# Performance work log

Hardware: AMD Instinct MI355X
Metric: run time of the kernel (lower is better)

## Reference

```python
import jax, jax.numpy as jnp
import numpy as np


def _pointnet(x, w1, b1, w2, b2, w3, b3):
    # x: [B, P, 5] -> pointwise MLP then max-pool over points -> [B, 64]
    h = jax.nn.relu(x @ w1.T + b1)
    h = jax.nn.relu(h @ w2.T + b2)
    h = h @ w3.T + b3
    return h.max(axis=1)


def _lstm_layer(x, wih, whh, bih, bhh):
    # x: [B, T, D]; PyTorch gate order i, f, g, o
    B = x.shape[0]
    H = whh.shape[1]
    def step(carry, xt):
        h, c = carry
        g = xt @ wih.T + bih + h @ whh.T + bhh
        i, f, gg, o = jnp.split(g, 4, axis=-1)
        c = jax.nn.sigmoid(f) * c + jax.nn.sigmoid(i) * jnp.tanh(gg)
        h = jax.nn.sigmoid(o) * jnp.tanh(c)
        return (h, c), h
    init = (jnp.zeros((B, H), x.dtype), jnp.zeros((B, H), x.dtype))
    (h_last, _), hs = jax.lax.scan(step, init, jnp.swapaxes(x, 0, 1))
    return jnp.swapaxes(hs, 0, 1), h_last


def _edge_conv(h, mask, wt, bt, wp, bp):
    # DGL EdgeConv: h_i' = max_{j in N(i)} theta(h_j - h_i) + phi(h_i)
    # theta is linear -> max_j (Th_j) - Th_i + b_theta + phi(h_i)
    Th = h @ wt.T                       # [V,128]
    Ph = h @ wp.T + bp                  # [V,128]
    neigh_max = jnp.max(jnp.where(mask[:, :, None], Th[None, :, :], -jnp.inf), axis=1)
    return neigh_max - Th + bt + Ph


def _edge_regr(e, w1, b1, w2, b2):
    return jax.nn.sigmoid(jax.nn.relu(e @ w1.T + b1) @ w2.T + b2)


def _affinity(h, N, M, er_w1, er_b1, er_w2, er_b2):
    # faithful to source: edges[i*M+j] = h[j] - h[i]  (j indexes first M rows, as in the code)
    E = (h[None, :M, :] - h[:N, None, :]).reshape(N * M, -1)
    return _edge_regr(E, er_w1, er_b1, er_w2, er_b2).reshape(N, M)


def setup_inputs() -> dict:
    key = jax.random.key(0)
    ks = iter(jax.random.split(key, 40))
    N, M, P, T = 256, 256, 512, 10
    lin = lambda k, o, i: (jax.random.normal(k, (o, i), jnp.float32) / np.sqrt(i)).astype(jnp.float32)
    inp = {
        'det_pts': jax.random.normal(next(ks), (N, P, 5), jnp.float32),
        'det_boxes': jax.random.normal(next(ks), (N, 9), jnp.float32),
        'track_pts': jax.random.normal(next(ks), (M, P, 5), jnp.float32),
        'track_boxes': jax.random.normal(next(ks), (M, T, 9), jnp.float32),
        'adj': jax.random.randint(next(ks), (N + M, N + M), 0, 2, jnp.int32),
        'pn_w1': lin(next(ks), 64, 5), 'pn_b1': jnp.zeros((64,), jnp.float32),
        'pn_w2': lin(next(ks), 128, 64), 'pn_b2': jnp.zeros((128,), jnp.float32),
        'pn_w3': lin(next(ks), 64, 128), 'pn_b3': jnp.zeros((64,), jnp.float32),
        'dm_w1': lin(next(ks), 32, 9), 'dm_b1': jnp.zeros((32,), jnp.float32),
        'dm_w2': lin(next(ks), 64, 32), 'dm_b2': jnp.zeros((64,), jnp.float32),
        'l0_wih': lin(next(ks), 256, 9), 'l0_whh': lin(next(ks), 256, 64),
        'l0_bih': jnp.zeros((256,), jnp.float32), 'l0_bhh': jnp.zeros((256,), jnp.float32),
        'l1_wih': lin(next(ks), 256, 64), 'l1_whh': lin(next(ks), 256, 64),
        'l1_bih': jnp.zeros((256,), jnp.float32), 'l1_bhh': jnp.zeros((256,), jnp.float32),
        'gc_wt': jnp.stack([lin(next(ks), 128, 128) for _ in range(4)]),
        'gc_bt': jnp.zeros((4, 128), jnp.float32),
        'gc_wp': jnp.stack([lin(next(ks), 128, 128) for _ in range(4)]),
        'gc_bp': jnp.zeros((4, 128), jnp.float32),
        'er_w1': lin(next(ks), 64, 128), 'er_b1': jnp.zeros((64,), jnp.float32),
        'er_w2': lin(next(ks), 1, 64), 'er_b2': jnp.zeros((1,), jnp.float32),
    }
    return inp


def reference(det_pts, det_boxes, track_pts, track_boxes, adj,
              pn_w1, pn_b1, pn_w2, pn_b2, pn_w3, pn_b3,
              dm_w1, dm_b1, dm_w2, dm_b2,
              l0_wih, l0_whh, l0_bih, l0_bhh,
              l1_wih, l1_whh, l1_bih, l1_bhh,
              gc_wt, gc_bt, gc_wp, gc_bp,
              er_w1, er_b1, er_w2, er_b2):
    N, M = det_pts.shape[0], track_pts.shape[0]
    V = N + M
    # appearance features (shared PointNet)
    det_app = _pointnet(det_pts, pn_w1, pn_b1, pn_w2, pn_b2, pn_w3, pn_b3)    # [N,64]
    trk_app = _pointnet(track_pts, pn_w1, pn_b1, pn_w2, pn_b2, pn_w3, pn_b3)  # [M,64]
    # motion features
    det_mot = jax.nn.relu(det_boxes @ dm_w1.T + dm_b1) @ dm_w2.T + dm_b2      # [N,64]
    hs0, _ = _lstm_layer(track_boxes, l0_wih, l0_whh, l0_bih, l0_bhh)
    _, trk_mot = _lstm_layer(hs0, l1_wih, l1_whh, l1_bih, l1_bhh)             # [M,64]
    h = jnp.concatenate([
        jnp.concatenate([det_app, det_mot], axis=1),
        jnp.concatenate([trk_app, trk_mot], axis=1)], axis=0)                 # [V,128]
    # neighbor-source mask: edge i->j for adj[i,j]!=0, plus self-loops
    mask = (adj.T != 0) | jnp.eye(V, dtype=bool)                              # mask[i,j]: j is source neighbor of i
    aff1 = None
    for k in range(4):
        h = jax.nn.relu(_edge_conv(h, mask, gc_wt[k], gc_bt[k], gc_wp[k], gc_bp[k]))
        if k == 0:
            aff1 = _affinity(h, N, M, er_w1, er_b1, er_w2, er_b2)
    aff_final = _affinity(h, N, M, er_w1, er_b1, er_w2, er_b2)
    return jnp.stack([aff1, aff_final])  # [2, N, M]
```

## Files before the change

kernel.cpp:

```cpp
#include <hip/hip_runtime.h>
#include <math.h>

#define NDET 256
#define NTRK 256
#define NV   512
#define PPTS 512

typedef short bf16x8 __attribute__((ext_vector_type(8)));
typedef float f32x4  __attribute__((ext_vector_type(4)));

__device__ __forceinline__ float sigf(float x) { return 1.f / (1.f + expf(-x)); }

__device__ __forceinline__ short f2bf(float f) {
    unsigned u = __float_as_uint(f);
    u += 0x7fffu + ((u >> 16) & 1u);
    return (short)(u >> 16);
}
__device__ __forceinline__ unsigned pack2bf(float lo, float hi) {
    return (unsigned)(unsigned short)f2bf(lo) | ((unsigned)(unsigned short)f2bf(hi) << 16);
}

__global__ __launch_bounds__(256) void pointnet_kernel(
    const float* __restrict__ det_pts, const float* __restrict__ track_pts,
    const float* __restrict__ w1, const float* __restrict__ b1,
    const float* __restrict__ w2, const float* __restrict__ b2,
    const float* __restrict__ w3, const float* __restrict__ b3,
    const float* __restrict__ det_boxes,
    const float* __restrict__ dw1, const float* __restrict__ db1,
    const float* __restrict__ dw2, const float* __restrict__ db2,
    float* __restrict__ hout)
{
    __shared__ __align__(16) short sW2[128][72];
    __shared__ __align__(16) short sW3[64][136];
    __shared__ __align__(16) short sH1[64][72];
    __shared__ __align__(16) short sH2[64][136];
    __shared__ __align__(16) float sX[320];
    __shared__ float sW1f[64][6];
    __shared__ float sB1[64];
    __shared__ float sbox[9];
    __shared__ float sh32[32];

    const int t  = threadIdx.x;
    const int b  = blockIdx.x;
    const int w  = t >> 6;
    const int ln = t & 15;
    const int kq = (t >> 4) & 3;
    const float* x = (b < NDET) ? (det_pts + (size_t)b * PPTS * 5)
                                : (track_pts + (size_t)(b - NDET) * PPTS * 5);

    for (int i = t; i < 8192; i += 256) sW2[i >> 6][i & 63] = f2bf(w2[i]);
    for (int i = t; i < 8192; i += 256) sW3[i >> 7][i & 127] = f2bf(w3[i]);
    for (int i = t; i < 320; i += 256) sW1f[i / 5][i % 5] = w1[i];
    if (t < 64) sB1[t] = b1[t];
    __syncthreads();

    bf16x8 bf2[2][2];
#pragma unroll
    for (int nt = 0; nt < 2; ++nt)
#pragma unroll
        for (int Kt = 0; Kt < 2; ++Kt)
            bf2[nt][Kt] = *(const bf16x8*)&sW2[32 * w + 16 * nt + ln][kq * 8 + 32 * Kt];
    bf16x8 bf3[4];
#pragma unroll
    for (int Kt = 0; Kt < 4; ++Kt)
        bf3[Kt] = *(const bf16x8*)&sW3[16 * w + ln][kq * 8 + 32 * Kt];
    float bn[2];
#pragma unroll
    for (int nt = 0; nt < 2; ++nt) bn[nt] = b2[32 * w + 16 * nt + ln];

    float runmax[4] = {-1e30f, -1e30f, -1e30f, -1e30f};

    const int pt = t & 63;
    for (int c = 0; c < PPTS / 64; ++c) {
        for (int i = t; i < 320; i += 256) sX[i] = x[c * 320 + i];
        __syncthreads();

        {
            float xv[5];
#pragma unroll
            for (int k = 0; k < 5; ++k) xv[k] = sX[pt * 5 + k];
#pragma unroll
            for (int jj = 0; jj < 8; ++jj) {
                const int d0 = w * 16 + 2 * jj;
                float a0 = sB1[d0], a1 = sB1[d0 + 1];
#pragma unroll
                for (int k = 0; k < 5; ++k) {
                    a0 = fmaf(xv[k], sW1f[d0][k], a0);
                    a1 = fmaf(xv[k], sW1f[d0 + 1][k], a1);
                }
                *(unsigned*)&sH1[pt][d0] = pack2bf(fmaxf(a0, 0.f), fmaxf(a1, 0.f));
            }
        }
        __syncthreads();

        {
            bf16x8 af[4][2];
#pragma unroll
            for (int Mt = 0; Mt < 4; ++Mt)
#pragma unroll
                for (int Kt = 0; Kt < 2; ++Kt)
                    af[Mt][Kt] = *(const bf16x8*)&sH1[16 * Mt + ln][kq * 8 + 32 * Kt];
#pragma unroll
            for (int Mt = 0; Mt < 4; ++Mt) {
#pragma unroll
                for (int nt = 0; nt < 2; ++nt) {
                    f32x4 cacc = {0.f, 0.f, 0.f, 0.f};
                    cacc = __builtin_amdgcn_mfma_f32_16x16x32_bf16(af[Mt][0], bf2[nt][0], cacc, 0, 0, 0);
                    cacc = __builtin_amdgcn_mfma_f32_16x16x32_bf16(af[Mt][1], bf2[nt][1], cacc, 0, 0, 0);
                    const int col = 32 * w + 16 * nt + ln;
#pragma unroll
                    for (int r = 0; r < 4; ++r)
                        sH2[16 * Mt + kq * 4 + r][col] = f2bf(fmaxf(cacc[r] + bn[nt], 0.f));
                }
            }
        }
        __syncthreads();

        {
#pragma unroll
            for (int Mt = 0; Mt < 4; ++Mt) {
                f32x4 cacc = {0.f, 0.f, 0.f, 0.f};
#pragma unroll
                for (int Kt = 0; Kt < 4; ++Kt) {
                    const bf16x8 a = *(const bf16x8*)&sH2[16 * Mt + ln][kq * 8 + 32 * Kt];
                    cacc = __builtin_amdgcn_mfma_f32_16x16x32_bf16(a, bf3[Kt], cacc, 0, 0, 0);
                }
#pragma unroll
                for (int r = 0; r < 4; ++r) runmax[r] = fmaxf(runmax[r], cacc[r]);
            }
        }
        __syncthreads();
    }

    float rm = fmaxf(fmaxf(runmax[0], runmax[1]), fmaxf(runmax[2], runmax[3]));
    rm = fmaxf(rm, __shfl_xor(rm, 16));
    rm = fmaxf(rm, __shfl_xor(rm, 32));
    if ((t & 63) < 16) {
        const int n = 16 * w + ln;
        hout[b * 128 + n] = rm + b3[n];
    }

    if (b < NDET) {
        if (t < 9) sbox[t] = det_boxes[b * 9 + t];
        __syncthreads();
        if (t < 32) {
            float a = db1[t];
#pragma unroll
            for (int k = 0; k < 9; ++k) a = fmaf(dw1[t * 9 + k], sbox[k], a);
            sh32[t] = fmaxf(a, 0.f);
        }
        __syncthreads();
        if (t < 64) {
            float a = db2[t];
#pragma unroll
            for (int k = 0; k < 32; ++k) a = fmaf(dw2[t * 32 + k], sh32[k], a);
            hout[b * 128 + 64 + t] = a;
        }
    }
}

__global__ __launch_bounds__(256, 1) void lstm_kernel(
    const float* __restrict__ track_boxes,
    const float* __restrict__ wih0, const float* __restrict__ whh0,
    const float* __restrict__ bih0, const float* __restrict__ bhh0,
    const float* __restrict__ wih1, const float* __restrict__ whh1,
    const float* __restrict__ bih1, const float* __restrict__ bhh1,
    float* __restrict__ hout)
{
    __shared__ float sx[90];
    __shared__ float sg[256];
    __shared__ __align__(16) float sh0[64];
    __shared__ __align__(16) float sh1[64];

    const int t = threadIdx.x;
    const int m = blockIdx.x;
    const int u = t & 63;

    if (t < 90) sx[t] = track_boxes[m * 90 + t];
    if (t < 64) { sh0[t] = 0.f; sh1[t] = 0.f; }

    float w0[9];
#pragma unroll
    for (int k = 0; k < 9; ++k) w0[k] = wih0[t * 9 + k];
    float4 wr0[16], wi1[16], wr1[16];
    {
        const float4* p0 = (const float4*)(whh0 + t * 64);
        const float4* p1 = (const float4*)(wih1 + t * 64);
        const float4* p2 = (const float4*)(whh1 + t * 64);
#pragma unroll
        for (int k = 0; k < 16; ++k) { wr0[k] = p0[k]; wi1[k] = p1[k]; wr1[k] = p2[k]; }
    }
    const float bias0 = bih0[t] + bhh0[t];
    const float bias1 = bih1[t] + bhh1[t];

    float c0 = 0.f, c1 = 0.f, h1reg = 0.f;
    __syncthreads();

    for (int s = 0; s < 10; ++s) {
        {
            float acc0 = bias0, acc1 = 0.f, acc2 = 0.f, acc3 = 0.f;
#pragma unroll
            for (int k = 0; k < 9; ++k) acc0 = fmaf(w0[k], sx[s * 9 + k], acc0);
            const float4* hv = (const float4*)sh0;
#pragma unroll
            for (int k = 0; k < 16; k += 4) {
                float4 hA = hv[k], hB = hv[k + 1], hC = hv[k + 2], hD = hv[k + 3];
                acc0 = fmaf(wr0[k].x, hA.x, acc0); acc0 = fmaf(wr0[k].y, hA.y, acc0);
                acc0 = fmaf(wr0[k].z, hA.z, acc0); acc0 = fmaf(wr0[k].w, hA.w, acc0);
                acc1 = fmaf(wr0[k+1].x, hB.x, acc1); acc1 = fmaf(wr0[k+1].y, hB.y, acc1);
                acc1 = fmaf(wr0[k+1].z, hB.z, acc1); acc1 = fmaf(wr0[k+1].w, hB.w, acc1);
                acc2 = fmaf(wr0[k+2].x, hC.x, acc2); acc2 = fmaf(wr0[k+2].y, hC.y, acc2);
                acc2 = fmaf(wr0[k+2].z, hC.z, acc2); acc2 = fmaf(wr0[k+2].w, hC.w, acc2);
                acc3 = fmaf(wr0[k+3].x, hD.x, acc3); acc3 = fmaf(wr0[k+3].y, hD.y, acc3);
                acc3 = fmaf(wr0[k+3].z, hD.z, acc3); acc3 = fmaf(wr0[k+3].w, hD.w, acc3);
            }
            sg[t] = (acc0 + acc1) + (acc2 + acc3);
        }
        __syncthreads();
        if (t < 64) {
            const float gi = sg[u], gf = sg[64 + u], gg = sg[128 + u], go = sg[192 + u];
            c0 = sigf(gf) * c0 + sigf(gi) * tanhf(gg);
            sh0[u] = sigf(go) * tanhf(c0);
        }
        __syncthreads();
        {
            float acc0 = bias1, acc1 = 0.f, acc2 = 0.f, acc3 = 0.f;
            const float4* xv = (const float4*)sh0;
            const float4* hv = (const float4*)sh1;
#pragma unroll
            for (int k = 0; k < 16; k += 4) {
                float4 xA = xv[k], xB = xv[k + 1], xC = xv[k + 2], xD = xv[k + 3];
                acc0 = fmaf(wi1[k].x, xA.x, acc0); acc0 = fmaf(wi1[k].y, xA.y, acc0);
                acc0 = fmaf(wi1[k].z, xA.z, acc0); acc0 = fmaf(wi1[k].w, xA.w, acc0);
                acc1 = fmaf(wi1[k+1].x, xB.x, acc1); acc1 = fmaf(wi1[k+1].y, xB.y, acc1);
                acc1 = fmaf(wi1[k+1].z, xB.z, acc1); acc1 = fmaf(wi1[k+1].w, xB.w, acc1);
                acc2 = fmaf(wi1[k+2].x, xC.x, acc2); acc2 = fmaf(wi1[k+2].y, xC.y, acc2);
                acc2 = fmaf(wi1[k+2].z, xC.z, acc2); acc2 = fmaf(wi1[k+2].w, xC.w, acc2);
                acc3 = fmaf(wi1[k+3].x, xD.x, acc3); acc3 = fmaf(wi1[k+3].y, xD.y, acc3);
                acc3 = fmaf(wi1[k+3].z, xD.z, acc3); acc3 = fmaf(wi1[k+3].w, xD.w, acc3);
            }
#pragma unroll
            for (int k = 0; k < 16; k += 4) {
                float4 hA = hv[k], hB = hv[k + 1], hC = hv[k + 2], hD = hv[k + 3];
                acc0 = fmaf(wr1[k].x, hA.x, acc0); acc0 = fmaf(wr1[k].y, hA.y, acc0);
                acc0 = fmaf(wr1[k].z, hA.z, acc0); acc0 = fmaf(wr1[k].w, hA.w, acc0);
                acc1 = fmaf(wr1[k+1].x, hB.x, acc1); acc1 = fmaf(wr1[k+1].y, hB.y, acc1);
                acc1 = fmaf(wr1[k+1].z, hB.z, acc1); acc1 = fmaf(wr1[k+1].w, hB.w, acc1);
                acc2 = fmaf(wr1[k+2].x, hC.x, acc2); acc2 = fmaf(wr1[k+2].y, hC.y, acc2);
                acc2 = fmaf(wr1[k+2].z, hC.z, acc2); acc2 = fmaf(wr1[k+2].w, hC.w, acc2);
                acc3 = fmaf(wr1[k+3].x, hD.x, acc3); acc3 = fmaf(wr1[k+3].y, hD.y, acc3);
                acc3 = fmaf(wr1[k+3].z, hD.z, acc3); acc3 = fmaf(wr1[k+3].w, hD.w, acc3);
            }
            sg[t] = (acc0 + acc1) + (acc2 + acc3);
        }
        __syncthreads();
        if (t < 64) {
            const float gi = sg[u], gf = sg[64 + u], gg = sg[128 + u], go = sg[192 + u];
            c1 = sigf(gf) * c1 + sigf(gi) * tanhf(gg);
            h1reg = sigf(go) * tanhf(c1);
            sh1[u] = h1reg;
        }
        __syncthreads();
    }

    if (t < 64) hout[(size_t)(NDET + m) * 128 + 64 + u] = h1reg;
}

__global__ __launch_bounds__(128) void econv_gemm_kernel(
    const float* __restrict__ hin, const float* __restrict__ wt,
    const float* __restrict__ wp, const float* __restrict__ bp,
    float* __restrict__ Th, float* __restrict__ Ph)
{
    __shared__ __align__(16) float srow[128];
    const int t = threadIdx.x, v = blockIdx.x;
    srow[t] = hin[v * 128 + t];
    __syncthreads();
    const float4* hr = (const float4*)srow;
    const float4* wtr = (const float4*)(wt + t * 128);
    const float4* wpr = (const float4*)(wp + t * 128);
    float aT = 0.f, aP = bp[t];
#pragma unroll 8
    for (int k = 0; k < 32; ++k) {
        const float4 h = hr[k];
        const float4 a = wtr[k];
        aT = fmaf(a.x, h.x, aT); aT = fmaf(a.y, h.y, aT);
        aT = fmaf(a.z, h.z, aT); aT = fmaf(a.w, h.w, aT);
        const float4 b = wpr[k];
        aP = fmaf(b.x, h.x, aP); aP = fmaf(b.y, h.y, aP);
        aP = fmaf(b.z, h.z, aP); aP = fmaf(b.w, h.w, aP);
    }
    Th[v * 128 + t] = aT;
    Ph[v * 128 + t] = aP;
}

__global__ __launch_bounds__(128) void econv_fused_kernel(
    const int* __restrict__ adj, const float* __restrict__ Th,
    const float* __restrict__ Ph, const float* __restrict__ bt,
    const float* __restrict__ wtn, const float* __restrict__ wpn,
    const float* __restrict__ bpn,
    const float* __restrict__ erw1, float* __restrict__ uu,
    float* __restrict__ Thn, float* __restrict__ Phn)
{
    __shared__ float sneg[NV];
    __shared__ __align__(16) float4 sred[4][32];
    __shared__ __align__(16) float sh[128];

    const int t = threadIdx.x, i = blockIdx.x;
    const int l32 = t & 31, grp = t >> 5;

    for (int j = t; j < NV; j += 128)
        sneg[j] = ((adj[j * NV + i] != 0) || (j == i)) ? 0.f : -3e38f;

    const float thi = Th[i * 128 + t];
    const float phi = Ph[i * 128 + t];
    const float btv = bt[t];
    __syncthreads();

    float4 mx = {-3e38f, -3e38f, -3e38f, -3e38f};
    const float* __restrict__ thp = Th + 4 * l32;
#pragma unroll 4
    for (int jb = 0; jb < NV; jb += 16) {
        float4 v[4];
#pragma unroll
        for (int jj = 0; jj < 4; ++jj)
            v[jj] = *(const float4*)&thp[(size_t)(jb + 4 * jj + grp) * 128];
#pragma unroll
        for (int jj = 0; jj < 4; ++jj) {
            const float s = sneg[jb + 4 * jj + grp];
            mx.x = fmaxf(mx.x, v[jj].x + s);
            mx.y = fmaxf(mx.y, v[jj].y + s);
            mx.z = fmaxf(mx.z, v[jj].z + s);
            mx.w = fmaxf(mx.w, v[jj].w + s);
        }
    }
    sred[grp][l32] = mx;
    __syncthreads();

    const float* rf = (const float*)sred;
    const float m = fmaxf(fmaxf(rf[t], rf[128 + t]), fmaxf(rf[256 + t], rf[384 + t]));
    sh[t] = fmaxf(m - thi + btv + phi, 0.f);
    __syncthreads();

    const float4* hr = (const float4*)sh;
    if (wtn) {
        const float4* wtr = (const float4*)(wtn + t * 128);
        const float4* wpr = (const float4*)(wpn + t * 128);
        float aT = 0.f, aP = bpn[t];
#pragma unroll 8
        for (int k = 0; k < 32; ++k) {
            const float4 h = hr[k];
            const float4 a = wtr[k];
            aT = fmaf(a.x, h.x, aT); aT = fmaf(a.y, h.y, aT);
            aT = fmaf(a.z, h.z, aT); aT = fmaf(a.w, h.w, aT);
            const float4 b = wpr[k];
            aP = fmaf(b.x, h.x, aP); aP = fmaf(b.y, h.y, aP);
            aP = fmaf(b.z, h.z, aP); aP = fmaf(b.w, h.w, aP);
        }
        Thn[i * 128 + t] = aT;
        Phn[i * 128 + t] = aP;
    }
    if (erw1 && i < NDET && t < 64) {
        const float4* wr = (const float4*)(erw1 + t * 128);
        float a = 0.f;
#pragma unroll 8
        for (int k = 0; k < 32; ++k) {
            const float4 h = hr[k], wv = wr[k];
            a = fmaf(wv.x, h.x, a); a = fmaf(wv.y, h.y, a);
            a = fmaf(wv.z, h.z, a); a = fmaf(wv.w, h.w, a);
        }
        uu[i * 64 + t] = a;
    }
}

__global__ __launch_bounds__(256) void edge_kernel(
    const float* __restrict__ u, const float* __restrict__ b1,
    const float* __restrict__ w2, const float* __restrict__ b2,
    float* __restrict__ out)
{
    __shared__ float sui[64], sw2[64], sb1[64];
    const int t = threadIdx.x, i = blockIdx.x;
    if (t < 64) { sui[t] = u[i * 64 + t]; sw2[t] = w2[t]; sb1[t] = b1[t]; }
    __syncthreads();
    const float4* ur = (const float4*)(u + t * 64);
    float a = b2[0];
#pragma unroll
    for (int k = 0; k < 16; ++k) {
        const float4 uv = ur[k];
        const int k4 = k * 4;
        a = fmaf(sw2[k4 + 0], fmaxf(uv.x - sui[k4 + 0] + sb1[k4 + 0], 0.f), a);
        a = fmaf(sw2[k4 + 1], fmaxf(uv.y - sui[k4 + 1] + sb1[k4 + 1], 0.f), a);
        a = fmaf(sw2[k4 + 2], fmaxf(uv.z - sui[k4 + 2] + sb1[k4 + 2], 0.f), a);
        a = fmaf(sw2[k4 + 3], fmaxf(uv.w - sui[k4 + 3] + sb1[k4 + 3], 0.f), a);
    }
    out[i * 256 + t] = 1.f / (1.f + expf(-a));
}

extern "C" void kernel_launch(void* const* d_in, const int* in_sizes, int n_in,
                              void* d_out, int out_size, void* d_ws, size_t ws_size,
                              hipStream_t stream)
{
    const float* det_pts     = (const float*)d_in[0];
    const float* det_boxes   = (const float*)d_in[1];
    const float* track_pts   = (const float*)d_in[2];
    const float* track_boxes = (const float*)d_in[3];
    const int*   adj         = (const int*)d_in[4];
    const float* pn_w1 = (const float*)d_in[5],  *pn_b1 = (const float*)d_in[6];
    const float* pn_w2 = (const float*)d_in[7],  *pn_b2 = (const float*)d_in[8];
    const float* pn_w3 = (const float*)d_in[9],  *pn_b3 = (const float*)d_in[10];
    const float* dm_w1 = (const float*)d_in[11], *dm_b1 = (const float*)d_in[12];
    const float* dm_w2 = (const float*)d_in[13], *dm_b2 = (const float*)d_in[14];
    const float* l0_wih = (const float*)d_in[15], *l0_whh = (const float*)d_in[16];
    const float* l0_bih = (const float*)d_in[17], *l0_bhh = (const float*)d_in[18];
    const float* l1_wih = (const float*)d_in[19], *l1_whh = (const float*)d_in[20];
    const float* l1_bih = (const float*)d_in[21], *l1_bhh = (const float*)d_in[22];
    const float* gc_wt = (const float*)d_in[23], *gc_bt = (const float*)d_in[24];
    const float* gc_wp = (const float*)d_in[25], *gc_bp = (const float*)d_in[26];
    const float* er_w1 = (const float*)d_in[27], *er_b1 = (const float*)d_in[28];
    const float* er_w2 = (const float*)d_in[29], *er_b2 = (const float*)d_in[30];
    float* out = (float*)d_out;

    float* hA  = (float*)d_ws;
    float* Th  = hA  + NV * 128;
    float* Ph  = Th  + NV * 128;
    float* Th2 = Ph  + NV * 128;
    float* Ph2 = Th2 + NV * 128;
    float* uu1 = Ph2 + NV * 128;
    float* uu2 = uu1 + NDET * 64;

    pointnet_kernel<<<NV, 256, 0, stream>>>(det_pts, track_pts,
        pn_w1, pn_b1, pn_w2, pn_b2, pn_w3, pn_b3,
        det_boxes, dm_w1, dm_b1, dm_w2, dm_b2, hA);
    lstm_kernel<<<NTRK, 256, 0, stream>>>(track_boxes,
        l0_wih, l0_whh, l0_bih, l0_bhh, l1_wih, l1_whh, l1_bih, l1_bhh, hA);

    econv_gemm_kernel<<<NV, 128, 0, stream>>>(hA,
        gc_wt, gc_wp, gc_bp, Th, Ph);

    const size_t WSZ = 128 * 128;
    econv_fused_kernel<<<NV, 128, 0, stream>>>(adj, Th, Ph, gc_bt,
        gc_wt + WSZ, gc_wp + WSZ, gc_bp + 128, er_w1, uu1, Th2, Ph2);
    econv_fused_kernel<<<NV, 128, 0, stream>>>(adj, Th2, Ph2, gc_bt + 128,
        gc_wt + 2 * WSZ, gc_wp + 2 * WSZ, gc_bp + 256, nullptr, nullptr, Th, Ph);
    econv_fused_kernel<<<NV, 128, 0, stream>>>(adj, Th, Ph, gc_bt + 256,
        gc_wt + 3 * WSZ, gc_wp + 3 * WSZ, gc_bp + 384, nullptr, nullptr, Th2, Ph2);
    econv_fused_kernel<<<NV, 128, 0, stream>>>(adj, Th2, Ph2, gc_bt + 384,
        nullptr, nullptr, nullptr, er_w1, uu2, nullptr, nullptr);

    edge_kernel<<<NDET, 256, 0, stream>>>(uu1, er_b1, er_w2, er_b2, out);
    edge_kernel<<<NDET, 256, 0, stream>>>(uu2, er_b1, er_w2, er_b2, out + NDET * NTRK);
}
```

Measured before the change: 246.4 us.

## Merge LSTM into PointNet kernel, batch edge-conv rows, merge edge kernels

Folds the LSTM into the PointNet launch as extra blocks so both run concurrently in one kernel. Edge-conv kernels now handle 4 destination nodes per block and stage Th tiles in shared memory, so each loaded neighbour row is reused across 4 nodes. The last layer is launched only for detection rows, and the two edge-regression launches become one. This cuts launch count and redundant global reads, at the cost of fewer blocks per edge-conv launch and heavier register and shared-memory pressure in the merged front kernel.

Result: slower. 317.1 us (+28.7%).

```diff
diff --git a/kernel.cpp b/kernel.cpp
--- a/kernel.cpp
+++ b/kernel.cpp
@@ -5,6 +5,7 @@
 #define NTRK 256
 #define NV   512
 #define PPTS 512
+#define IB   4
 
 typedef short bf16x8 __attribute__((ext_vector_type(8)));
 typedef float f32x4  __attribute__((ext_vector_type(4)));
@@ -20,7 +21,7 @@
     return (unsigned)(unsigned short)f2bf(lo) | ((unsigned)(unsigned short)f2bf(hi) << 16);
 }
 
-__global__ __launch_bounds__(256) void pointnet_kernel(
+__global__ __launch_bounds__(256, 2) void front_kernel(
     const float* __restrict__ det_pts, const float* __restrict__ track_pts,
     const float* __restrict__ w1, const float* __restrict__ b1,
     const float* __restrict__ w2, const float* __restrict__ b2,
@@ -28,6 +29,11 @@
     const float* __restrict__ det_boxes,
     const float* __restrict__ dw1, const float* __restrict__ db1,
     const float* __restrict__ dw2, const float* __restrict__ db2,
+    const float* __restrict__ track_boxes,
+    const float* __restrict__ wih0, const float* __restrict__ whh0,
+    const float* __restrict__ bih0, const float* __restrict__ bhh0,
+    const float* __restrict__ wih1, const float* __restrict__ whh1,
+    const float* __restrict__ bih1, const float* __restrict__ bhh1,
     float* __restrict__ hout)
 {
     __shared__ __align__(16) short sW2[128][72];
@@ -39,9 +45,108 @@
     __shared__ float sB1[64];
     __shared__ float sbox[9];
     __shared__ float sh32[32];
-
-    const int t  = threadIdx.x;
-    const int b  = blockIdx.x;
+    __shared__ float lx[90];
+    __shared__ float lg[256];
+    __shared__ __align__(16) float lh0[64];
+    __shared__ __align__(16) float lh1[64];
+
+    const int t = threadIdx.x;
+
+    if (blockIdx.x < NTRK) {
+        const int m = blockIdx.x;
+        const int u = t & 63;
+
+        if (t < 90) lx[t] = track_boxes[m * 90 + t];
+        if (t < 64) { lh0[t] = 0.f; lh1[t] = 0.f; }
+
+        float w0[9];
+#pragma unroll
+        for (int k = 0; k < 9; ++k) w0[k] = wih0[t * 9 + k];
+        float4 wr0[16], wi1[16], wr1[16];
+        {
+            const float4* p0 = (const float4*)(whh0 + t * 64);
+            const float4* p1 = (const float4*)(wih1 + t * 64);
+            const float4* p2 = (const float4*)(whh1 + t * 64);
+#pragma unroll
+            for (int k = 0; k < 16; ++k) { wr0[k] = p0[k]; wi1[k] = p1[k]; wr1[k] = p2[k]; }
+        }
+        const float bias0 = bih0[t] + bhh0[t];
+        const float bias1 = bih1[t] + bhh1[t];
+
+        float c0 = 0.f, c1 = 0.f, h1reg = 0.f;
+        __syncthreads();
+
+        for (int s = 0; s < 10; ++s) {
+            {
+                float acc0 = bias0, acc1 = 0.f, acc2 = 0.f, acc3 = 0.f;
+#pragma unroll
+                for (int k = 0; k < 9; ++k) acc0 = fmaf(w0[k], lx[s * 9 + k], acc0);
+                const float4* hv = (const float4*)lh0;
+#pragma unroll
+                for (int k = 0; k < 16; k += 4) {
+                    float4 hA = hv[k], hB = hv[k + 1], hC = hv[k + 2], hD = hv[k + 3];
+                    acc0 = fmaf(wr0[k].x, hA.x, acc0); acc0 = fmaf(wr0[k].y, hA.y, acc0);
+                    acc0 = fmaf(wr0[k].z, hA.z, acc0); acc0 = fmaf(wr0[k].w, hA.w, acc0);
+                    acc1 = fmaf(wr0[k+1].x, hB.x, acc1); acc1 = fmaf(wr0[k+1].y, hB.y, acc1);
+                    acc1 = fmaf(wr0[k+1].z, hB.z, acc1); acc1 = fmaf(wr0[k+1].w, hB.w, acc1);
+                    acc2 = fmaf(wr0[k+2].x, hC.x, acc2); acc2 = fmaf(wr0[k+2].y, hC.y, acc2);
+                    acc2 = fmaf(wr0[k+2].z, hC.z, acc2); acc2 = fmaf(wr0[k+2].w, hC.w, acc2);
+                    acc3 = fmaf(wr0[k+3].x, hD.x, acc3); acc3 = fmaf(wr0[k+3].y, hD.y, acc3);
+                    acc3 = fmaf(wr0[k+3].z, hD.z, acc3); acc3 = fmaf(wr0[k+3].w, hD.w, acc3);
+                }
+                lg[t] = (acc0 + acc1) + (acc2 + acc3);
+            }
+            __syncthreads();
+            if (t < 64) {
+                const float gi = lg[u], gf = lg[64 + u], gg = lg[128 + u], go = lg[192 + u];
+                c0 = sigf(gf) * c0 + sigf(gi) * tanhf(gg);
+                lh0[u] = sigf(go) * tanhf(c0);
+            }
+            __syncthreads();
+            {
+                float acc0 = bias1, acc1 = 0.f, acc2 = 0.f, acc3 = 0.f;
+                const float4* xv = (const float4*)lh0;
+                const float4* hv = (const float4*)lh1;
+#pragma unroll
+                for (int k = 0; k < 16; k += 4) {
+                    float4 xA = xv[k], xB = xv[k + 1], xC = xv[k + 2], xD = xv[k + 3];
+                    acc0 = fmaf(wi1[k].x, xA.x, acc0); acc0 = fmaf(wi1[k].y, xA.y, acc0);
+                    acc0 = fmaf(wi1[k].z, xA.z, acc0); acc0 = fmaf(wi1[k].w, xA.w, acc0);
+                    acc1 = fmaf(wi1[k+1].x, xB.x, acc1); acc1 = fmaf(wi1[k+1].y, xB.y, acc1);
+                    acc1 = fmaf(wi1[k+1].z, xB.z, acc1); acc1 = fmaf(wi1[k+1].w, xB.w, acc1);
+                    acc2 = fmaf(wi1[k+2].x, xC.x, acc2); acc2 = fmaf(wi1[k+2].y, xC.y, acc2);
+                    acc2 = fmaf(wi1[k+2].z, xC.z, acc2); acc2 = fmaf(wi1[k+2].w, xC.w, acc2);
+                    acc3 = fmaf(wi1[k+3].x, xD.x, acc3); acc3 = fmaf(wi1[k+3].y, xD.y, acc3);
+                    acc3 = fmaf(wi1[k+3].z, xD.z, acc3); acc3 = fmaf(wi1[k+3].w, xD.w, acc3);
+                }
+#pragma unroll
+                for (int k = 0; k < 16; k += 4) {
+                    float4 hA = hv[k], hB = hv[k + 1], hC = hv[k + 2], hD = hv[k + 3];
+                    acc0 = fmaf(wr1[k].x, hA.x, acc0); acc0 = fmaf(wr1[k].y, hA.y, acc0);
+                    acc0 = fmaf(wr1[k].z, hA.z, acc0); acc0 = fmaf(wr1[k].w, hA.w, acc0);
+                    acc1 = fmaf(wr1[k+1].x, hB.x, acc1); acc1 = fmaf(wr1[k+1].y, hB.y, acc1);
+                    acc1 = fmaf(wr1[k+1].z, hB.z, acc1); acc1 = fmaf(wr1[k+1].w, hB.w, acc1);
+                    acc2 = fmaf(wr1[k+2].x, hC.x, acc2); acc2 = fmaf(wr1[k+2].y, hC.y, acc2);
+                    acc2 = fmaf(wr1[k+2].z, hC.z, acc2); acc2 = fmaf(wr1[k+2].w, hC.w, acc2);
+                    acc3 = fmaf(wr1[k+3].x, hD.x, acc3); acc3 = fmaf(wr1[k+3].y, hD.y, acc3);
+                    acc3 = fmaf(wr1[k+3].z, hD.z, acc3); acc3 = fmaf(wr1[k+3].w, hD.w, acc3);
+                }
+                lg[t] = (acc0 + acc1) + (acc2 + acc3);
+            }
+            __syncthreads();
+            if (t < 64) {
+                const float gi = lg[u], gf = lg[64 + u], gg = lg[128 + u], go = lg[192 + u];
+                c1 = sigf(gf) * c1 + sigf(gi) * tanhf(gg);
+                h1reg = sigf(go) * tanhf(c1);
+                lh1[u] = h1reg;
+            }
+            __syncthreads();
+        }
+        if (t < 64) hout[(size_t)(NDET + m) * 128 + 64 + u] = h1reg;
+        return;
+    }
+
+    const int b  = blockIdx.x - NTRK;
     const int w  = t >> 6;
     const int ln = t & 15;
     const int kq = (t >> 4) & 3;
@@ -74,7 +179,6 @@
     for (int c = 0; c < PPTS / 64; ++c) {
         for (int i = t; i < 320; i += 256) sX[i] = x[c * 320 + i];
         __syncthreads();
-
         {
             float xv[5];
 #pragma unroll
@@ -92,7 +196,6 @@
             }
         }
         __syncthreads();
-
         {
             bf16x8 af[4][2];
 #pragma unroll
@@ -115,7 +218,6 @@
             }
         }
         __syncthreads();
-
         {
 #pragma unroll
             for (int Mt = 0; Mt < 4; ++Mt) {
@@ -159,141 +261,45 @@
     }
 }
 
-__global__ __launch_bounds__(256, 1) void lstm_kernel(
-    const float* __restrict__ track_boxes,
-    const float* __restrict__ wih0, const float* __restrict__ whh0,
-    const float* __restrict__ bih0, const float* __restrict__ bhh0,
-    const float* __restrict__ wih1, const float* __restrict__ whh1,
-    const float* __restrict__ bih1, const float* __restrict__ bhh1,
-    float* __restrict__ hout)
-{
-    __shared__ float sx[90];
-    __shared__ float sg[256];
-    __shared__ __align__(16) float sh0[64];
-    __shared__ __align__(16) float sh1[64];
-
-    const int t = threadIdx.x;
-    const int m = blockIdx.x;
-    const int u = t & 63;
-
-    if (t < 90) sx[t] = track_boxes[m * 90 + t];
-    if (t < 64) { sh0[t] = 0.f; sh1[t] = 0.f; }
-
-    float w0[9];
-#pragma unroll
-    for (int k = 0; k < 9; ++k) w0[k] = wih0[t * 9 + k];
-    float4 wr0[16], wi1[16], wr1[16];
-    {
-        const float4* p0 = (const float4*)(whh0 + t * 64);
-        const float4* p1 = (const float4*)(wih1 + t * 64);
-        const float4* p2 = (const float4*)(whh1 + t * 64);
-#pragma unroll
-        for (int k = 0; k < 16; ++k) { wr0[k] = p0[k]; wi1[k] = p1[k]; wr1[k] = p2[k]; }
-    }
-    const float bias0 = bih0[t] + bhh0[t];
-    const float bias1 = bih1[t] + bhh1[t];
-
-    float c0 = 0.f, c1 = 0.f, h1reg = 0.f;
-    __syncthreads();
-
-    for (int s = 0; s < 10; ++s) {
-        {
-            float acc0 = bias0, acc1 = 0.f, acc2 = 0.f, acc3 = 0.f;
-#pragma unroll
-            for (int k = 0; k < 9; ++k) acc0 = fmaf(w0[k], sx[s * 9 + k], acc0);
-            const float4* hv = (const float4*)sh0;
-#pragma unroll
-            for (int k = 0; k < 16; k += 4) {
-                float4 hA = hv[k], hB = hv[k + 1], hC = hv[k + 2], hD = hv[k + 3];
-                acc0 = fmaf(wr0[k].x, hA.x, acc0); acc0 = fmaf(wr0[k].y, hA.y, acc0);
-                acc0 = fmaf(wr0[k].z, hA.z, acc0); acc0 = fmaf(wr0[k].w, hA.w, acc0);
-                acc1 = fmaf(wr0[k+1].x, hB.x, acc1); acc1 = fmaf(wr0[k+1].y, hB.y, acc1);
-                acc1 = fmaf(wr0[k+1].z, hB.z, acc1); acc1 = fmaf(wr0[k+1].w, hB.w, acc1);
-                acc2 = fmaf(wr0[k+2].x, hC.x, acc2); acc2 = fmaf(wr0[k+2].y, hC.y, acc2);
-                acc2 = fmaf(wr0[k+2].z, hC.z, acc2); acc2 = fmaf(wr0[k+2].w, hC.w, acc2);
-                acc3 = fmaf(wr0[k+3].x, hD.x, acc3); acc3 = fmaf(wr0[k+3].y, hD.y, acc3);
-                acc3 = fmaf(wr0[k+3].z, hD.z, acc3); acc3 = fmaf(wr0[k+3].w, hD.w, acc3);
-            }
-            sg[t] = (acc0 + acc1) + (acc2 + acc3);
-        }
-        __syncthreads();
-        if (t < 64) {
-            const float gi = sg[u], gf = sg[64 + u], gg = sg[128 + u], go = sg[192 + u];
-            c0 = sigf(gf) * c0 + sigf(gi) * tanhf(gg);
-            sh0[u] = sigf(go) * tanhf(c0);
-        }
-        __syncthreads();
-        {
-            float acc0 = bias1, acc1 = 0.f, acc2 = 0.f, acc3 = 0.f;
-            const float4* xv = (const float4*)sh0;
-            const float4* hv = (const float4*)sh1;
-#pragma unroll
-            for (int k = 0; k < 16; k += 4) {
-                float4 xA = xv[k], xB = xv[k + 1], xC = xv[k + 2], xD = xv[k + 3];
-                acc0 = fmaf(wi1[k].x, xA.x, acc0); acc0 = fmaf(wi1[k].y, xA.y, acc0);
-                acc0 = fmaf(wi1[k].z, xA.z, acc0); acc0 = fmaf(wi1[k].w, xA.w, acc0);
-                acc1 = fmaf(wi1[k+1].x, xB.x, acc1); acc1 = fmaf(wi1[k+1].y, xB.y, acc1);
-                acc1 = fmaf(wi1[k+1].z, xB.z, acc1); acc1 = fmaf(wi1[k+1].w, xB.w, acc1);
-                acc2 = fmaf(wi1[k+2].x, xC.x, acc2); acc2 = fmaf(wi1[k+2].y, xC.y, acc2);
-                acc2 = fmaf(wi1[k+2].z, xC.z, acc2); acc2 = fmaf(wi1[k+2].w, xC.w, acc2);
-                acc3 = fmaf(wi1[k+3].x, xD.x, acc3); acc3 = fmaf(wi1[k+3].y, xD.y, acc3);
-                acc3 = fmaf(wi1[k+3].z, xD.z, acc3); acc3 = fmaf(wi1[k+3].w, xD.w, acc3);
-            }
-#pragma unroll
-            for (int k = 0; k < 16; k += 4) {
-                float4 hA = hv[k], hB = hv[k + 1], hC = hv[k + 2], hD = hv[k + 3];
-                acc0 = fmaf(wr1[k].x, hA.x, acc0); acc0 = fmaf(wr1[k].y, hA.y, acc0);
-                acc0 = fmaf(wr1[k].z, hA.z, acc0); acc0 = fmaf(wr1[k].w, hA.w, acc0);
-                acc1 = fmaf(wr1[k+1].x, hB.x, acc1); acc1 = fmaf(wr1[k+1].y, hB.y, acc1);
-                acc1 = fmaf(wr1[k+1].z, hB.z, acc1); acc1 = fmaf(wr1[k+1].w, hB.w, acc1);
-                acc2 = fmaf(wr1[k+2].x, hC.x, acc2); acc2 = fmaf(wr1[k+2].y, hC.y, acc2);
-                acc2 = fmaf(wr1[k+2].z, hC.z, acc2); acc2 = fmaf(wr1[k+2].w, hC.w, acc2);
-                acc3 = fmaf(wr1[k+3].x, hD.x, acc3); acc3 = fmaf(wr1[k+3].y, hD.y, acc3);
-                acc3 = fmaf(wr1[k+3].z, hD.z, acc3); acc3 = fmaf(wr1[k+3].w, hD.w, acc3);
-            }
-            sg[t] = (acc0 + acc1) + (acc2 + acc3);
-        }
-        __syncthreads();
-        if (t < 64) {
-            const float gi = sg[u], gf = sg[64 + u], gg = sg[128 + u], go = sg[192 + u];
-            c1 = sigf(gf) * c1 + sigf(gi) * tanhf(gg);
-            h1reg = sigf(go) * tanhf(c1);
-            sh1[u] = h1reg;
-        }
-        __syncthreads();
-    }
-
-    if (t < 64) hout[(size_t)(NDET + m) * 128 + 64 + u] = h1reg;
-}
-
-__global__ __launch_bounds__(128) void econv_gemm_kernel(
+__global__ __launch_bounds__(256) void econv_gemm_kernel(
     const float* __restrict__ hin, const float* __restrict__ wt,
     const float* __restrict__ wp, const float* __restrict__ bp,
     float* __restrict__ Th, float* __restrict__ Ph)
 {
-    __shared__ __align__(16) float srow[128];
-    const int t = threadIdx.x, v = blockIdx.x;
-    srow[t] = hin[v * 128 + t];
-    __syncthreads();
-    const float4* hr = (const float4*)srow;
-    const float4* wtr = (const float4*)(wt + t * 128);
-    const float4* wpr = (const float4*)(wp + t * 128);
-    float aT = 0.f, aP = bp[t];
+    __shared__ __align__(16) float sh[IB][128];
+    const int t = threadIdx.x, i0 = blockIdx.x * IB;
+    for (int idx = t; idx < IB * 128; idx += 256) sh[idx >> 7][idx & 127] = hin[i0 * 128 + idx];
+    __syncthreads();
+
+    const int is = t >> 6, n2 = (t & 63) * 2;
+    const float4* hr = (const float4*)sh[is];
+    const float4* wA = (const float4*)(wt + (size_t)n2 * 128);
+    const float4* wB = (const float4*)(wt + (size_t)(n2 + 1) * 128);
+    const float4* pA = (const float4*)(wp + (size_t)n2 * 128);
+    const float4* pB = (const float4*)(wp + (size_t)(n2 + 1) * 128);
+    float t0 = 0.f, t1 = 0.f, p0 = bp[n2], p1 = bp[n2 + 1];
 #pragma unroll 8
     for (int k = 0; k < 32; ++k) {
         const float4 h = hr[k];
-        const float4 a = wtr[k];
-        aT = fmaf(a.x, h.x, aT); aT = fmaf(a.y, h.y, aT);
-        aT = fmaf(a.z, h.z, aT); aT = fmaf(a.w, h.w, aT);
-        const float4 b = wpr[k];
-        aP = fmaf(b.x, h.x, aP); aP = fmaf(b.y, h.y, aP);
-        aP = fmaf(b.z, h.z, aP); aP = fmaf(b.w, h.w, aP);
-    }
-    Th[v * 128 + t] = aT;
-    Ph[v * 128 + t] = aP;
-}
-
-__global__ __launch_bounds__(128) void econv_fused_kernel(
+        const float4 a = wA[k];
+        t0 = fmaf(a.x, h.x, t0); t0 = fmaf(a.y, h.y, t0);
+        t0 = fmaf(a.z, h.z, t0); t0 = fmaf(a.w, h.w, t0);
+        const float4 b = wB[k];
+        t1 = fmaf(b.x, h.x, t1); t1 = fmaf(b.y, h.y, t1);
+        t1 = fmaf(b.z, h.z, t1); t1 = fmaf(b.w, h.w, t1);
+        const float4 c = pA[k];
+        p0 = fmaf(c.x, h.x, p0); p0 = fmaf(c.y, h.y, p0);
+        p0 = fmaf(c.z, h.z, p0); p0 = fmaf(c.w, h.w, p0);
+        const float4 d = pB[k];
+        p1 = fmaf(d.x, h.x, p1); p1 = fmaf(d.y, h.y, p1);
+        p1 = fmaf(d.z, h.z, p1); p1 = fmaf(d.w, h.w, p1);
+    }
+    float2 tv = {t0, t1}, pv = {p0, p1};
+    *(float2*)&Th[(size_t)(i0 + is) * 128 + n2] = tv;
+    *(float2*)&Ph[(size_t)(i0 + is) * 128 + n2] = pv;
+}
+
+__global__ __launch_bounds__(256) void econv_fused_kernel(
     const int* __restrict__ adj, const float* __restrict__ Th,
     const float* __restrict__ Ph, const float* __restrict__ bt,
     const float* __restrict__ wtn, const float* __restrict__ wpn,
@@ -301,66 +307,105 @@
     const float* __restrict__ erw1, float* __restrict__ uu,
     float* __restrict__ Thn, float* __restrict__ Phn)
 {
-    __shared__ float sneg[NV];
-    __shared__ __align__(16) float4 sred[4][32];
-    __shared__ __align__(16) float sh[128];
-
-    const int t = threadIdx.x, i = blockIdx.x;
-    const int l32 = t & 31, grp = t >> 5;
-
-    for (int j = t; j < NV; j += 128)
-        sneg[j] = ((adj[j * NV + i] != 0) || (j == i)) ? 0.f : -3e38f;
-
-    const float thi = Th[i * 128 + t];
-    const float phi = Ph[i * 128 + t];
-    const float btv = bt[t];
-    __syncthreads();
-
-    float4 mx = {-3e38f, -3e38f, -3e38f, -3e38f};
-    const float* __restrict__ thp = Th + 4 * l32;
-#pragma unroll 4
-    for (int jb = 0; jb < NV; jb += 16) {
-        float4 v[4];
-#pragma unroll
-        for (int jj = 0; jj < 4; ++jj)
-            v[jj] = *(const float4*)&thp[(size_t)(jb + 4 * jj + grp) * 128];
-#pragma unroll
-        for (int jj = 0; jj < 4; ++jj) {
-            const float s = sneg[jb + 4 * jj + grp];
-            mx.x = fmaxf(mx.x, v[jj].x + s);
-            mx.y = fmaxf(mx.y, v[jj].y + s);
-            mx.z = fmaxf(mx.z, v[jj].z + s);
-            mx.w = fmaxf(mx.w, v[jj].w + s);
-        }
-    }
-    sred[grp][l32] = mx;
-    __syncthreads();
-
-    const float* rf = (const float*)sred;
-    const float m = fmaxf(fmaxf(rf[t], rf[128 + t]), fmaxf(rf[256 + t], rf[384 + t]));
-    sh[t] = fmaxf(m - thi + btv + phi, 0.f);
-    __syncthreads();
-
-    const float4* hr = (const float4*)sh;
+    __shared__ __align__(16) float4 sneg[NV];
+    __shared__ __align__(16) float sTh[64][132];
+    __shared__ __align__(16) float4 sred[8][IB][32];
+    __shared__ __align__(16) float sh[IB][128];
+
+    const int t = threadIdx.x, i0 = blockIdx.x * IB;
+    const int q = t & 31, jgrp = t >> 5;
+
+    for (int idx = t; idx < IB * NV; idx += 256) {
+        const int j = idx >> 2, is = idx & 3;
+        ((float*)&sneg[j])[is] =
+            ((adj[j * NV + i0 + is] != 0) || (j == i0 + is)) ? 0.f : -3e38f;
+    }
+    __syncthreads();
+
+    float4 mx[IB];
+#pragma unroll
+    for (int is = 0; is < IB; ++is) { mx[is].x = -3e38f; mx[is].y = -3e38f; mx[is].z = -3e38f; mx[is].w = -3e38f; }
+
+    for (int jb = 0; jb < NV; jb += 64) {
+        for (int idx = t; idx < 64 * 32; idx += 256) {
+            const int r = idx >> 5, c = idx & 31;
+            *(float4*)&sTh[r][4 * c] = *(const float4*)&Th[(size_t)(jb + r) * 128 + 4 * c];
+        }
+        __syncthreads();
+#pragma unroll
+        for (int jj = 0; jj < 8; ++jj) {
+            const int j = jgrp * 8 + jj;
+            const float4 v = *(const float4*)&sTh[j][4 * q];
+            const float4 s4 = sneg[jb + j];
+            mx[0].x = fmaxf(mx[0].x, v.x + s4.x); mx[0].y = fmaxf(mx[0].y, v.y + s4.x);
+            mx[0].z = fmaxf(mx[0].z, v.z + s4.x); mx[0].w = fmaxf(mx[0].w, v.w + s4.x);
+            mx[1].x = fmaxf(mx[1].x, v.x + s4.y); mx[1].y = fmaxf(mx[1].y, v.y + s4.y);
+            mx[1].z = fmaxf(mx[1].z, v.z + s4.y); mx[1].w = fmaxf(mx[1].w, v.w + s4.y);
+            mx[2].x = fmaxf(mx[2].x, v.x + s4.z); mx[2].y = fmaxf(mx[2].y, v.y + s4.z);
+            mx[2].z = fmaxf(mx[2].z, v.z + s4.z); mx[2].w = fmaxf(mx[2].w, v.w + s4.z);
+            mx[3].x = fmaxf(mx[3].x, v.x + s4.w); mx[3].y = fmaxf(mx[3].y, v.y + s4.w);
+            mx[3].z = fmaxf(mx[3].z, v.z + s4.w); mx[3].w = fmaxf(mx[3].w, v.w + s4.w);
+        }
+        __syncthreads();
+    }
+#pragma unroll
+    for (int is = 0; is < IB; ++is) sred[jgrp][is][q] = mx[is];
+    __syncthreads();
+
+    if (t < 128) {
+        const int is = t >> 5, qq = t & 31;
+        float4 m = sred[0][is][qq];
+#pragma unroll
+        for (int jg = 1; jg < 8; ++jg) {
+            const float4 r = sred[jg][is][qq];
+            m.x = fmaxf(m.x, r.x); m.y = fmaxf(m.y, r.y);
+            m.z = fmaxf(m.z, r.z); m.w = fmaxf(m.w, r.w);
+        }
+        const int row = i0 + is;
+        const float4 thi = *(const float4*)&Th[(size_t)row * 128 + 4 * qq];
+        const float4 phi = *(const float4*)&Ph[(size_t)row * 128 + 4 * qq];
+        const float4 btv = *(const float4*)&bt[4 * qq];
+        float4 hv;
+        hv.x = fmaxf(m.x - thi.x + btv.x + phi.x, 0.f);
+        hv.y = fmaxf(m.y - thi.y + btv.y + phi.y, 0.f);
+        hv.z = fmaxf(m.z - thi.z + btv.z + phi.z, 0.f);
+        hv.w = fmaxf(m.w - thi.w + btv.w + phi.w, 0.f);
+        *(float4*)&sh[is][4 * qq] = hv;
+    }
+    __syncthreads();
+
     if (wtn) {
-        const float4* wtr = (const float4*)(wtn + t * 128);
-        const float4* wpr = (const float4*)(wpn + t * 128);
-        float aT = 0.f, aP = bpn[t];
+        const int is = t >> 6, n2 = (t & 63) * 2;
+        const float4* hr = (const float4*)sh[is];
+        const float4* wA = (const float4*)(wtn + (size_t)n2 * 128);
+        const float4* wB = (const float4*)(wtn + (size_t)(n2 + 1) * 128);
+        const float4* pA = (const float4*)(wpn + (size_t)n2 * 128);
+        const float4* pB = (const float4*)(wpn + (size_t)(n2 + 1) * 128);
+        float t0 = 0.f, t1 = 0.f, p0 = bpn[n2], p1 = bpn[n2 + 1];
 #pragma unroll 8
         for (int k = 0; k < 32; ++k) {
             const float4 h = hr[k];
-            const float4 a = wtr[k];
-            aT = fmaf(a.x, h.x, aT); aT = fmaf(a.y, h.y, aT);
-            aT = fmaf(a.z, h.z, aT); aT = fmaf(a.w, h.w, aT);
-            const float4 b = wpr[k];
-            aP = fmaf(b.x, h.x, aP); aP = fmaf(b.y, h.y, aP);
-            aP = fmaf(b.z, h.z, aP); aP = fmaf(b.w, h.w, aP);
-        }
-        Thn[i * 128 + t] = aT;
-        Phn[i * 128 + t] = aP;
-    }
-    if (erw1 && i < NDET && t < 64) {
-        const float4* wr = (const float4*)(erw1 + t * 128);
+            const float4 a = wA[k];
+            t0 = fmaf(a.x, h.x, t0); t0 = fmaf(a.y, h.y, t0);
+            t0 = fmaf(a.z, h.z, t0); t0 = fmaf(a.w, h.w, t0);
+            const float4 b = wB[k];
+            t1 = fmaf(b.x, h.x, t1); t1 = fmaf(b.y, h.y, t1);
+            t1 = fmaf(b.z, h.z, t1); t1 = fmaf(b.w, h.w, t1);
+            const float4 c = pA[k];
+            p0 = fmaf(c.x, h.x, p0); p0 = fmaf(c.y, h.y, p0);
+            p0 = fmaf(c.z, h.z, p0); p0 = fmaf(c.w, h.w, p0);
+            const float4 d = pB[k];
+            p1 = fmaf(d.x, h.x, p1); p1 = fmaf(d.y, h.y, p1);
+            p1 = fmaf(d.z, h.z, p1); p1 = fmaf(d.w, h.w, p1);
+        }
+        float2 tv = {t0, t1}, pv = {p0, p1};
+        *(float2*)&Thn[(size_t)(i0 + is) * 128 + n2] = tv;
+        *(float2*)&Phn[(size_t)(i0 + is) * 128 + n2] = pv;
+    }
+    if (erw1 && i0 < NDET) {
+        const int is = t >> 6, n = t & 63;
+        const float4* hr = (const float4*)sh[is];
+        const float4* wr = (const float4*)(erw1 + (size_t)n * 128);
         float a = 0.f;
 #pragma unroll 8
         for (int k = 0; k < 32; ++k) {
@@ -368,17 +413,20 @@
             a = fmaf(wv.x, h.x, a); a = fmaf(wv.y, h.y, a);
             a = fmaf(wv.z, h.z, a); a = fmaf(wv.w, h.w, a);
         }
-        uu[i * 64 + t] = a;
+        uu[(size_t)(i0 + is) * 64 + n] = a;
     }
 }
 
 __global__ __launch_bounds__(256) void edge_kernel(
-    const float* __restrict__ u, const float* __restrict__ b1,
-    const float* __restrict__ w2, const float* __restrict__ b2,
-    float* __restrict__ out)
+    const float* __restrict__ uu1, const float* __restrict__ uu2,
+    const float* __restrict__ b1, const float* __restrict__ w2,
+    const float* __restrict__ b2, float* __restrict__ out)
 {
     __shared__ float sui[64], sw2[64], sb1[64];
-    const int t = threadIdx.x, i = blockIdx.x;
+    const int t = threadIdx.x, blk = blockIdx.x;
+    const float* u = (blk < NDET) ? uu1 : uu2;
+    float* o = (blk < NDET) ? out : out + NDET * NTRK;
+    const int i = blk & (NDET - 1);
     if (t < 64) { sui[t] = u[i * 64 + t]; sw2[t] = w2[t]; sb1[t] = b1[t]; }
     __syncthreads();
     const float4* ur = (const float4*)(u + t * 64);
@@ -392,7 +440,7 @@
         a = fmaf(sw2[k4 + 2], fmaxf(uv.z - sui[k4 + 2] + sb1[k4 + 2], 0.f), a);
         a = fmaf(sw2[k4 + 3], fmaxf(uv.w - sui[k4 + 3] + sb1[k4 + 3], 0.f), a);
     }
-    out[i * 256 + t] = 1.f / (1.f + expf(-a));
+    o[i * 256 + t] = 1.f / (1.f + expf(-a));
 }
 
 extern "C" void kernel_launch(void* const* d_in, const int* in_sizes, int n_in,
@@ -427,25 +475,23 @@
     float* uu1 = Ph2 + NV * 128;
     float* uu2 = uu1 + NDET * 64;
 
-    pointnet_kernel<<<NV, 256, 0, stream>>>(det_pts, track_pts,
+    front_kernel<<<NTRK + NV, 256, 0, stream>>>(det_pts, track_pts,
         pn_w1, pn_b1, pn_w2, pn_b2, pn_w3, pn_b3,
-        det_boxes, dm_w1, dm_b1, dm_w2, dm_b2, hA);
-    lstm_kernel<<<NTRK, 256, 0, stream>>>(track_boxes,
-        l0_wih, l0_whh, l0_bih, l0_bhh, l1_wih, l1_whh, l1_bih, l1_bhh, hA);
-
-    econv_gemm_kernel<<<NV, 128, 0, stream>>>(hA,
-        gc_wt, gc_wp, gc_bp, Th, Ph);
+        det_boxes, dm_w1, dm_b1, dm_w2, dm_b2,
+        track_boxes, l0_wih, l0_whh, l0_bih, l0_bhh,
+        l1_wih, l1_whh, l1_bih, l1_bhh, hA);
+
+    econv_gemm_kernel<<<NV / IB, 256, 0, stream>>>(hA, gc_wt, gc_wp, gc_bp, Th, Ph);
 
     const size_t WSZ = 128 * 128;
-    econv_fused_kernel<<<NV, 128, 0, stream>>>(adj, Th, Ph, gc_bt,
+    econv_fused_kernel<<<NV / IB, 256, 0, stream>>>(adj, Th, Ph, gc_bt,
         gc_wt + WSZ, gc_wp + WSZ, gc_bp + 128, er_w1, uu1, Th2, Ph2);
-    econv_fused_kernel<<<NV, 128, 0, stream>>>(adj, Th2, Ph2, gc_bt + 128,
+    econv_fused_kernel<<<NV / IB, 256, 0, stream>>>(adj, Th2, Ph2, gc_bt + 128,
         gc_wt + 2 * WSZ, gc_wp + 2 * WSZ, gc_bp + 256, nullptr, nullptr, Th, Ph);
-    econv_fused_kernel<<<NV, 128, 0, stream>>>(adj, Th, Ph, gc_bt + 256,
+    econv_fused_kernel<<<NV / IB, 256, 0, stream>>>(adj, Th, Ph, gc_bt + 256,
         gc_wt + 3 * WSZ, gc_wp + 3 * WSZ, gc_bp + 384, nullptr, nullptr, Th2, Ph2);
-    econv_fused_kernel<<<NV, 128, 0, stream>>>(adj, Th2, Ph2, gc_bt + 384,
+    econv_fused_kernel<<<NDET / IB, 256, 0, stream>>>(adj, Th2, Ph2, gc_bt + 384,
         nullptr, nullptr, nullptr, er_w1, uu2, nullptr, nullptr);
 
-    edge_kernel<<<NDET, 256, 0, stream>>>(uu1, er_b1, er_w2, er_b2, out);
-    edge_kernel<<<NDET, 256, 0, stream>>>(uu2, er_b1, er_w2, er_b2, out + NDET * NTRK);
-}
+    edge_kernel<<<NV, 256, 0, stream>>>(uu1, uu2, er_b1, er_w2, er_b2, out);
+}
```
